# Optimization experiments

Measured on AMD Instinct MI355X. Metric: run time of the kernel, lower is better.

The kernel has to match this reference:

```python
import jax, jax.numpy as jnp
import numpy as np

N_NODES = 50000
N_EDGES = 500000
IN_FEATS = 64
HIDDEN = 64
OUT_FEATS = 8
N_LAYERS = 6
NEG_SLOPE = 0.2
LN_EPS = 1e-5


def setup_inputs() -> dict:
    key = jax.random.key(0)
    ks = jax.random.split(key, 12)
    s_in = 1.0 / np.sqrt(IN_FEATS)
    s_h = 1.0 / np.sqrt(HIDDEN)
    return {
        "nodes": jax.random.normal(ks[0], (N_NODES, IN_FEATS), jnp.float32),
        "src": jax.random.randint(ks[1], (N_EDGES,), 0, N_NODES, jnp.int32),
        "dst": jax.random.randint(ks[2], (N_EDGES,), 0, N_NODES, jnp.int32),
        "w_in": jax.random.normal(ks[3], (IN_FEATS, HIDDEN), jnp.float32) * s_in,
        "b_in": jnp.zeros((HIDDEN,), jnp.float32),
        "w_src": jax.random.normal(ks[4], (N_LAYERS, HIDDEN, HIDDEN), jnp.float32) * s_h,
        "b_src": jnp.zeros((N_LAYERS, HIDDEN), jnp.float32),
        "w_dst": jax.random.normal(ks[5], (N_LAYERS, HIDDEN, HIDDEN), jnp.float32) * s_h,
        "b_dst": jnp.zeros((N_LAYERS, HIDDEN), jnp.float32),
        "attn": jax.random.normal(ks[6], (N_LAYERS, HIDDEN), jnp.float32) * s_h,
        "gamma": jnp.ones((N_LAYERS, HIDDEN), jnp.float32),
        "beta": jnp.zeros((N_LAYERS, HIDDEN), jnp.float32),
        "w_out": jax.random.normal(ks[7], (HIDDEN, OUT_FEATS), jnp.float32) * s_h,
        "b_out": jnp.zeros((OUT_FEATS,), jnp.float32),
    }


def _layernorm(x, g, b):
    m = jnp.mean(x, axis=-1, keepdims=True)
    v = jnp.mean(jnp.square(x - m), axis=-1, keepdims=True)
    return (x - m) * jax.lax.rsqrt(v + LN_EPS) * g + b


def _gatv2(h, src, dst, ws, bs, wd, bd, a, n_nodes):
    # GATv2Conv, num_heads=1 (DGL semantics)
    fs = h @ ws + bs                                  # [N, H] fc_src
    fd = h @ wd + bd                                  # [N, H] fc_dst
    e = jax.nn.leaky_relu(fs[src] + fd[dst], NEG_SLOPE)  # [E, H]
    score = e @ a                                     # [E]
    # segment softmax over incoming edges of each dst node
    mx = jax.ops.segment_max(score, dst, num_segments=n_nodes)
    ex = jnp.exp(score - mx[dst])
    denom = jax.ops.segment_sum(ex, dst, num_segments=n_nodes)
    alpha = ex / denom[dst]                           # [E]
    return jax.ops.segment_sum(alpha[:, None] * fs[src], dst, num_segments=n_nodes)


def reference(nodes, src, dst, w_in, b_in, w_src, b_src, w_dst, b_dst, attn, gamma, beta, w_out, b_out):
    n = nodes.shape[0]
    h = nodes @ w_in + b_in
    for i in range(N_LAYERS):
        t = _gatv2(h, src, dst, w_src[i], b_src[i], w_dst[i], b_dst[i], attn[i], n)
        t = _layernorm(t, gamma[i], beta[i])
        h = h + jax.nn.gelu(t, approximate=False)
    return h @ w_out + b_out
```

## Files before the change

kernel.cpp:

```cpp
#include <hip/hip_runtime.h>
#include <math.h>

#define N_NODES 50000
#define N_EDGES 500000
#define NLAYERS 6
#define NEG_SLOPE 0.2f
#define LN_EPS 1e-5f
#define SCAN_B 1024
#define NSCAN_BLOCKS ((N_NODES + SCAN_B - 1) / SCAN_B)
#define LOG2E 1.4426950408889634f

typedef __attribute__((ext_vector_type(8))) short short8;
typedef __attribute__((ext_vector_type(4))) float f32x4;

__device__ __forceinline__ float wave_sum64(float v) {
#pragma unroll
    for (int m = 32; m >= 1; m >>= 1) v += __shfl_xor(v, m, 64);
    return v;
}

__device__ __forceinline__ int wave_incl_scan(int v, int lane) {
#pragma unroll
    for (int offs = 1; offs < 64; offs <<= 1) {
        int t = __shfl_up(v, offs, 64);
        if (lane >= offs) v += t;
    }
    return v;
}

__device__ __forceinline__ unsigned bf16_rne(float v) {
    unsigned u = __float_as_uint(v);
    return (u + 0x7fffu + ((u >> 16) & 1u)) >> 16;
}

__device__ __forceinline__ float fast_exp2(float x) {
    float r;
    asm("v_exp_f32 %0, %1" : "=v"(r) : "v"(x));
    return r;
}

__global__ void count_deg(const int* __restrict__ dst, int* __restrict__ deg,
                          int* __restrict__ hist) {
    if (blockIdx.x == 0 && threadIdx.x < 64) hist[threadIdx.x] = 0;
    int i = blockIdx.x * blockDim.x + threadIdx.x;
    if (i < N_EDGES) atomicAdd(&deg[dst[i]], 1);
}

__global__ void scan1(const int* __restrict__ deg, int* __restrict__ row_ptr,
                      int* __restrict__ bsum, int* __restrict__ hist) {
    __shared__ int lhist[64];
    __shared__ int wtot[16];
    int t = threadIdx.x;
    if (t < 64) lhist[t] = 0;
    int i = blockIdx.x * SCAN_B + t;
    int lane = t & 63, wv = t >> 6;
    int v = (i < N_NODES) ? deg[i] : 0;
    __syncthreads();
    if (i < N_NODES) atomicAdd(&lhist[min(v, 63)], 1);
    int incl = wave_incl_scan(v, lane);
    if (lane == 63) wtot[wv] = incl;
    __syncthreads();
    if (wv == 0) {
        int wval = (lane < 16) ? wtot[lane] : 0;
        int ws = wave_incl_scan(wval, lane);
        if (lane < 16) wtot[lane] = ws - wval;
    }
    __syncthreads();
    int excl = incl - v + wtot[wv];
    if (i < N_NODES) row_ptr[i] = excl;
    if (t == SCAN_B - 1) bsum[blockIdx.x] = excl + v;
    if (t < 64) atomicAdd(&hist[t], lhist[t]);
}

__global__ void scan3(int* __restrict__ row_ptr, const int* __restrict__ bsum,
                      int* __restrict__ pos, const int* __restrict__ hist,
                      int* __restrict__ binpos) {
    __shared__ int boff_s;
    int t = threadIdx.x;
    if (t < 64) {
        int v = (t < NSCAN_BLOCKS && t < (int)blockIdx.x) ? bsum[t] : 0;
#pragma unroll
        for (int m = 32; m >= 1; m >>= 1) v += __shfl_xor(v, m, 64);
        if (t == 0) boff_s = v;
    }
    if (blockIdx.x == 0 && t >= 64 && t < 128) {
        int lane = t - 64;
        int v = hist[lane];
        int incl = wave_incl_scan(v, lane);
        binpos[lane] = incl - v;
    }
    __syncthreads();
    int i = blockIdx.x * SCAN_B + t;
    if (i < N_NODES) {
        int r = row_ptr[i] + boff_s;
        row_ptr[i] = r;
        pos[i] = r;
    }
    if (i == 0) row_ptr[N_NODES] = N_EDGES;
}

__global__ void bucket_nodes(const int* __restrict__ deg, int* __restrict__ binpos,
                             int* __restrict__ perm) {
    __shared__ int lhist[64], lbase[64];
    int t = threadIdx.x;
    if (t < 64) lhist[t] = 0;
    __syncthreads();
    int i = blockIdx.x * SCAN_B + t;
    int b = 0;
    if (i < N_NODES) {
        b = min(deg[i], 63);
        atomicAdd(&lhist[b], 1);
    }
    __syncthreads();
    if (t < 64) {
        lbase[t] = atomicAdd(&binpos[t], lhist[t]);
        lhist[t] = 0;
    }
    __syncthreads();
    if (i < N_NODES) {
        int r = atomicAdd(&lhist[b], 1);
        perm[lbase[b] + r] = i;
    }
}

__global__ void scatter_edges(const int* __restrict__ dst, const int* __restrict__ src,
                              int* __restrict__ pos, int* __restrict__ srcs) {
    int i = blockIdx.x * blockDim.x + threadIdx.x;
    if (i < N_EDGES) {
        int p = atomicAdd(&pos[dst[i]], 1);
        srcs[p] = src[i];
    }
}

__global__ void pack_w(const float* __restrict__ w_in, const float* __restrict__ w_src,
                       const float* __restrict__ w_dst, unsigned short* __restrict__ wpk_hi,
                       unsigned short* __restrict__ wpk_lo) {
    int b = blockIdx.x;
    const float* W = (b == 0) ? w_in
                              : (b <= 6 ? w_src + (size_t)(b - 1) * 4096
                                        : w_dst + (size_t)(b - 7) * 4096);
    unsigned short* hi = wpk_hi + (size_t)b * 4096;
    unsigned short* lo = wpk_lo + (size_t)b * 4096;
    for (int idx = threadIdx.x; idx < 4096; idx += 256) {
        int t = idx >> 10;
        int s = (idx >> 9) & 1;
        int l = (idx >> 3) & 63;
        int j = idx & 7;
        int row = s * 32 + (l >> 4) * 8 + j;
        int col = t * 16 + (l & 15);
        float v = W[row * 64 + col];
        unsigned rh = bf16_rne(v);
        float hf = __uint_as_float(rh << 16);
        unsigned rl = bf16_rne(v - hf);
        hi[idx] = (unsigned short)rh;
        lo[idx] = (unsigned short)rl;
    }
}

__device__ __forceinline__ void load_split8(const float* __restrict__ p, short8& hi, short8& lo) {
    float4 x0 = *(const float4*)p;
    float4 x1 = *(const float4*)(p + 4);
    float v[8] = {x0.x, x0.y, x0.z, x0.w, x1.x, x1.y, x1.z, x1.w};
#pragma unroll
    for (int j = 0; j < 8; ++j) {
        unsigned rh = bf16_rne(v[j]);
        float hf = __uint_as_float(rh << 16);
        unsigned rl = bf16_rne(v[j] - hf);
        hi[j] = (short)rh;
        lo[j] = (short)rl;
    }
}

__device__ __forceinline__ void mfma_16rows(const short8 ah0, const short8 ah1, const short8 al0,
                                            const short8 al1,
                                            const unsigned short* __restrict__ whi,
                                            const unsigned short* __restrict__ wlo, int lane,
                                            f32x4 acc[4]) {
#pragma unroll
    for (int t = 0; t < 4; ++t) {
#pragma unroll
        for (int s = 0; s < 2; ++s) {
            const size_t boff = ((size_t)((t * 2 + s) * 64 + lane)) * 8;
            short8 bh = *(const short8*)(whi + boff);
            short8 bl = *(const short8*)(wlo + boff);
            short8 a_h = s ? ah1 : ah0;
            short8 a_l = s ? al1 : al0;
            acc[t] = __builtin_amdgcn_mfma_f32_16x16x32_bf16(a_h, bh, acc[t], 0, 0, 0);
            acc[t] = __builtin_amdgcn_mfma_f32_16x16x32_bf16(a_l, bh, acc[t], 0, 0, 0);
            acc[t] = __builtin_amdgcn_mfma_f32_16x16x32_bf16(a_h, bl, acc[t], 0, 0, 0);
        }
    }
}

__global__ void mfma_in_proj(const float* __restrict__ X, const unsigned short* __restrict__ whi,
                             const unsigned short* __restrict__ wlo,
                             const float* __restrict__ bias, float* __restrict__ H) {
    int lane = threadIdx.x & 63, wv = threadIdx.x >> 6;
    int R = blockIdx.x * 64 + wv * 16;
    int arow = min(R + (lane & 15), N_NODES - 1);
    const float* p = X + (size_t)arow * 64 + (lane >> 4) * 8;
    short8 ah0, ah1, al0, al1;
    load_split8(p, ah0, al0);
    load_split8(p + 32, ah1, al1);
    f32x4 acc[4];
    f32x4 z = {0.f, 0.f, 0.f, 0.f};
#pragma unroll
    for (int t = 0; t < 4; ++t) acc[t] = z;
    mfma_16rows(ah0, ah1, al0, al1, whi, wlo, lane, acc);
    int crow = R + (lane >> 4) * 4;
#pragma unroll
    for (int t = 0; t < 4; ++t) {
        int col = t * 16 + (lane & 15);
        float bv = bias[col];
#pragma unroll
        for (int r = 0; r < 4; ++r) {
            int row = crow + r;
            if (row < N_NODES) H[(size_t)row * 64 + col] = acc[t][r] + bv;
        }
    }
}

__global__ void mfma_dual(const float* __restrict__ X, const unsigned short* __restrict__ wshi,
                          const unsigned short* __restrict__ wslo, const float* __restrict__ bs,
                          const unsigned short* __restrict__ wdhi,
                          const unsigned short* __restrict__ wdlo, const float* __restrict__ bd,
                          float* __restrict__ FS, float* __restrict__ FD) {
    int lane = threadIdx.x & 63, wv = threadIdx.x >> 6;
    int R = blockIdx.x * 64 + wv * 16;
    int arow = min(R + (lane & 15), N_NODES - 1);
    const float* p = X + (size_t)arow * 64 + (lane >> 4) * 8;
    short8 ah0, ah1, al0, al1;
    load_split8(p, ah0, al0);
    load_split8(p + 32, ah1, al1);
    f32x4 accS[4], accD[4];
    f32x4 z = {0.f, 0.f, 0.f, 0.f};
#pragma unroll
    for (int t = 0; t < 4; ++t) {
        accS[t] = z;
        accD[t] = z;
    }
    mfma_16rows(ah0, ah1, al0, al1, wshi, wslo, lane, accS);
    mfma_16rows(ah0, ah1, al0, al1, wdhi, wdlo, lane, accD);
    int crow = R + (lane >> 4) * 4;
#pragma unroll
    for (int t = 0; t < 4; ++t) {
        int col = t * 16 + (lane & 15);
        float bsv = bs[col], bdv = bd[col];
#pragma unroll
        for (int r = 0; r < 4; ++r) {
            int row = crow + r;
            if (row < N_NODES) {
                FS[(size_t)row * 64 + col] = accS[t][r] + bsv;
                FD[(size_t)row * 64 + col] = accD[t][r] + bdv;
            }
        }
    }
}

#define WPB 4
__global__ void node_fused_kernel(const float* __restrict__ fs, const float* __restrict__ fd,
                                  const int* __restrict__ row_ptr, const int* __restrict__ srcs,
                                  const int* __restrict__ perm, const float* __restrict__ attn,
                                  const float* __restrict__ gamma, const float* __restrict__ beta,
                                  float* __restrict__ h) {
    __shared__ float xpose[WPB][64];
    int lane = threadIdx.x & 63;
    int wv = threadIdx.x >> 6;
    int q = lane >> 4;
    int ql = lane & 15;
    int f0 = ql << 2;
    int idx = blockIdx.x * WPB + wv;
    if (idx >= N_NODES) return;
    int n = perm[idx];
    float gL = gamma[lane], bL = beta[lane];
    float hval = h[(size_t)n * 64 + lane];
    float4 a4 = *(const float4*)&attn[f0];
    a4.x *= LOG2E;
    a4.y *= LOG2E;
    a4.z *= LOG2E;
    a4.w *= LOG2E;
    int beg = row_ptr[n], end = row_ptr[n + 1];
    int deg = end - beg;
    float4 fd4 = *(const float4*)&fd[(size_t)n * 64 + f0];
    float d = 0.f;
    float4 acc = make_float4(0.f, 0.f, 0.f, 0.f);
    for (int c0 = 0; c0 < deg; c0 += 64) {
        int cl = min(64, deg - c0);
        int sv = (lane < cl) ? srcs[beg + c0 + lane] : 0;
        int nt = (cl + 3) >> 2;
        float4 rowA = make_float4(0.f, 0.f, 0.f, 0.f), rowB = rowA;
        int sid0 = __shfl(sv, q, 64);
        if (q < cl) rowA = *(const float4*)&fs[(size_t)sid0 * 64 + f0];
        int sid1 = __shfl(sv, (4 + q) & 63, 64);
        if (4 + q < cl) rowB = *(const float4*)&fs[(size_t)sid1 * 64 + f0];
        for (int t = 0; t < nt; ++t) {
            int eoff = 4 * t + q;
            bool valid = eoff < cl;
            float4 cur = rowA;
            rowA = rowB;
            int e2 = 4 * (t + 2) + q;
            int sid2 = __shfl(sv, e2 & 63, 64);
            if (e2 < cl) rowB = *(const float4*)&fs[(size_t)sid2 * 64 + f0];
            float vx = cur.x + fd4.x, vy = cur.y + fd4.y;
            float vz = cur.z + fd4.z, vw = cur.w + fd4.w;
            vx = fmaxf(vx, NEG_SLOPE * vx);
            vy = fmaxf(vy, NEG_SLOPE * vy);
            vz = fmaxf(vz, NEG_SLOPE * vz);
            vw = fmaxf(vw, NEG_SLOPE * vw);
            float sp = fmaf(a4.x, vx, fmaf(a4.y, vy, fmaf(a4.z, vz, a4.w * vw)));
            sp += __shfl_xor(sp, 1, 64);
            sp += __shfl_xor(sp, 2, 64);
            sp += __shfl_xor(sp, 4, 64);
            sp += __shfl_xor(sp, 8, 64);
            float w = valid ? fast_exp2(sp) : 0.f;
            d += w;
            acc.x = fmaf(w, cur.x, acc.x);
            acc.y = fmaf(w, cur.y, acc.y);
            acc.z = fmaf(w, cur.z, acc.z);
            acc.w = fmaf(w, cur.w, acc.w);
        }
    }
    d += __shfl_xor(d, 16, 64);
    d += __shfl_xor(d, 32, 64);
    acc.x += __shfl_xor(acc.x, 16, 64);
    acc.y += __shfl_xor(acc.y, 16, 64);
    acc.z += __shfl_xor(acc.z, 16, 64);
    acc.w += __shfl_xor(acc.w, 16, 64);
    acc.x += __shfl_xor(acc.x, 32, 64);
    acc.y += __shfl_xor(acc.y, 32, 64);
    acc.z += __shfl_xor(acc.z, 32, 64);
    acc.w += __shfl_xor(acc.w, 32, 64);
    float inv = (d > 0.f) ? 1.f / d : 0.f;
    acc.x *= inv;
    acc.y *= inv;
    acc.z *= inv;
    acc.w *= inv;
    if (q == 0) *(float4*)&xpose[wv][f0] = acc;
    float val = xpose[wv][lane];
    float mean = wave_sum64(val) * 0.015625f;
    float dev = val - mean;
    float var = wave_sum64(dev * dev) * 0.015625f;
    float rstd = rsqrtf(var + LN_EPS);
    float tval = fmaf(dev * rstd, gL, bL);
    float g = 0.5f * tval * (1.f + erff(tval * 0.70710678118654752f));
    h[(size_t)n * 64 + lane] = hval + g;
}

__global__ void out_proj_kernel(const float* __restrict__ h, const float* __restrict__ W,
                                const float* __restrict__ b, float* __restrict__ out) {
    __shared__ float Ws[64 * 8];
    __shared__ float bs[8];
    __shared__ float Hs[32][65];
    int t = threadIdx.x;
    for (int i = t; i < 512; i += 256) Ws[i] = W[i];
    if (t < 8) bs[t] = b[t];
    int n0 = blockIdx.x * 32;
    for (int i = t; i < 32 * 64; i += 256) {
        int r = i >> 6, c = i & 63;
        int n = n0 + r;
        Hs[r][c] = (n < N_NODES) ? h[(size_t)n * 64 + c] : 0.f;
    }
    __syncthreads();
    int nl = t >> 3, o = t & 7;
    int n = n0 + nl;
    if (n >= N_NODES) return;
    float acc = bs[o];
#pragma unroll
    for (int k = 0; k < 64; ++k) acc = fmaf(Hs[nl][k], Ws[k * 8 + o], acc);
    out[(size_t)n * 8 + o] = acc;
}

extern "C" void kernel_launch(void* const* d_in, const int* in_sizes, int n_in,
                              void* d_out, int out_size, void* d_ws, size_t ws_size,
                              hipStream_t stream) {
    const float* nodes = (const float*)d_in[0];
    const int* src = (const int*)d_in[1];
    const int* dst = (const int*)d_in[2];
    const float* w_in = (const float*)d_in[3];
    const float* b_in = (const float*)d_in[4];
    const float* w_src = (const float*)d_in[5];
    const float* b_src = (const float*)d_in[6];
    const float* w_dst = (const float*)d_in[7];
    const float* b_dst = (const float*)d_in[8];
    const float* attn = (const float*)d_in[9];
    const float* gamma = (const float*)d_in[10];
    const float* beta = (const float*)d_in[11];
    const float* w_out = (const float*)d_in[12];
    const float* b_out = (const float*)d_in[13];
    float* out = (float*)d_out;

    char* ws = (char*)d_ws;
    size_t off = 0;
    auto alloc = [&](size_t bytes) {
        void* p = ws + off;
        off += (bytes + 255) & ~(size_t)255;
        return p;
    };
    float* h = (float*)alloc((size_t)N_NODES * 64 * 4);
    float* fs = (float*)alloc((size_t)N_NODES * 64 * 4);
    float* fd = (float*)alloc((size_t)N_NODES * 64 * 4);
    unsigned short* wpk_hi = (unsigned short*)alloc((size_t)13 * 4096 * 2);
    unsigned short* wpk_lo = (unsigned short*)alloc((size_t)13 * 4096 * 2);
    int* deg = (int*)alloc((size_t)N_NODES * 4);
    int* row_ptr = (int*)alloc((size_t)(N_NODES + 1) * 4);
    int* pos = (int*)alloc((size_t)N_NODES * 4);
    int* srcs = (int*)alloc((size_t)N_EDGES * 4);
    int* bsum = (int*)alloc((size_t)NSCAN_BLOCKS * 4);
    int* hist = (int*)alloc((size_t)64 * 4);
    int* binpos = (int*)alloc((size_t)64 * 4);
    int* perm = (int*)alloc((size_t)N_NODES * 4);

    hipMemsetAsync(deg, 0, (size_t)N_NODES * 4, stream);
    count_deg<<<(N_EDGES + 255) / 256, 256, 0, stream>>>(dst, deg, hist);
    scan1<<<NSCAN_BLOCKS, SCAN_B, 0, stream>>>(deg, row_ptr, bsum, hist);
    scan3<<<NSCAN_BLOCKS, SCAN_B, 0, stream>>>(row_ptr, bsum, pos, hist, binpos);
    bucket_nodes<<<NSCAN_BLOCKS, SCAN_B, 0, stream>>>(deg, binpos, perm);
    scatter_edges<<<(N_EDGES + 255) / 256, 256, 0, stream>>>(dst, src, pos, srcs);

    pack_w<<<13, 256, 0, stream>>>(w_in, w_src, w_dst, wpk_hi, wpk_lo);

    mfma_in_proj<<<(N_NODES + 63) / 64, 256, 0, stream>>>(nodes, wpk_hi, wpk_lo, b_in, h);

    for (int l = 0; l < NLAYERS; ++l) {
        mfma_dual<<<(N_NODES + 63) / 64, 256, 0, stream>>>(
            h, wpk_hi + (size_t)(1 + l) * 4096, wpk_lo + (size_t)(1 + l) * 4096,
            b_src + (size_t)l * 64, wpk_hi + (size_t)(7 + l) * 4096,
            wpk_lo + (size_t)(7 + l) * 4096, b_dst + (size_t)l * 64, fs, fd);
        node_fused_kernel<<<(N_NODES + WPB - 1) / WPB, 256, 0, stream>>>(
            fs, fd, row_ptr, srcs, perm, attn + (size_t)l * 64, gamma + (size_t)l * 64,
            beta + (size_t)l * 64, h);
    }

    out_proj_kernel<<<(N_NODES + 31) / 32, 256, 0, stream>>>(h, w_out, b_out, out);
}
```

Before: 352.5 us.

## Process two degree-sorted nodes per wave with DPP row reductions

```diff
diff --git a/kernel.cpp b/kernel.cpp
--- a/kernel.cpp
+++ b/kernel.cpp
@@ -16,6 +16,29 @@
 __device__ __forceinline__ float wave_sum64(float v) {
 #pragma unroll
     for (int m = 32; m >= 1; m >>= 1) v += __shfl_xor(v, m, 64);
+    return v;
+}
+
+__device__ __forceinline__ float dpp_rowsum16(float v) {
+    int x = __float_as_int(v);
+    int y = __builtin_amdgcn_update_dpp(x, x, 0x121, 0xf, 0xf, false);
+    v += __int_as_float(y);
+    x = __float_as_int(v);
+    y = __builtin_amdgcn_update_dpp(x, x, 0x122, 0xf, 0xf, false);
+    v += __int_as_float(y);
+    x = __float_as_int(v);
+    y = __builtin_amdgcn_update_dpp(x, x, 0x124, 0xf, 0xf, false);
+    v += __int_as_float(y);
+    x = __float_as_int(v);
+    y = __builtin_amdgcn_update_dpp(x, x, 0x128, 0xf, 0xf, false);
+    v += __int_as_float(y);
+    return v;
+}
+
+__device__ __forceinline__ float wave_sum64_fast(float v) {
+    v = dpp_rowsum16(v);
+    v += __shfl_xor(v, 16, 64);
+    v += __shfl_xor(v, 32, 64);
     return v;
 }
 
@@ -56,7 +79,7 @@
     int lane = t & 63, wv = t >> 6;
     int v = (i < N_NODES) ? deg[i] : 0;
     __syncthreads();
-    if (i < N_NODES) atomicAdd(&lhist[min(v, 63)], 1);
+    if (i < N_NODES) atomicAdd(&lhist[63 - min(v, 63)], 1);
     int incl = wave_incl_scan(v, lane);
     if (lane == 63) wtot[wv] = incl;
     __syncthreads();
@@ -108,7 +131,7 @@
     int i = blockIdx.x * SCAN_B + t;
     int b = 0;
     if (i < N_NODES) {
-        b = min(deg[i], 63);
+        b = 63 - min(deg[i], 63);
         atomicAdd(&lhist[b], 1);
     }
     __syncthreads();
@@ -263,87 +286,131 @@
                                   const int* __restrict__ perm, const float* __restrict__ attn,
                                   const float* __restrict__ gamma, const float* __restrict__ beta,
                                   float* __restrict__ h) {
-    __shared__ float xpose[WPB][64];
+    __shared__ float xpose[WPB][2][64];
     int lane = threadIdx.x & 63;
     int wv = threadIdx.x >> 6;
     int q = lane >> 4;
     int ql = lane & 15;
     int f0 = ql << 2;
-    int idx = blockIdx.x * WPB + wv;
-    if (idx >= N_NODES) return;
-    int n = perm[idx];
+    int gw = blockIdx.x * WPB + wv;
+    int iA = gw * 2;
+    if (iA >= N_NODES) return;
+    int iB = iA + 1;
+    bool hasB = iB < N_NODES;
+    int nA = perm[iA];
+    int nB = hasB ? perm[iB] : nA;
     float gL = gamma[lane], bL = beta[lane];
-    float hval = h[(size_t)n * 64 + lane];
+    float hvalA = h[(size_t)nA * 64 + lane];
+    float hvalB = h[(size_t)nB * 64 + lane];
     float4 a4 = *(const float4*)&attn[f0];
     a4.x *= LOG2E;
     a4.y *= LOG2E;
     a4.z *= LOG2E;
     a4.w *= LOG2E;
-    int beg = row_ptr[n], end = row_ptr[n + 1];
-    int deg = end - beg;
-    float4 fd4 = *(const float4*)&fd[(size_t)n * 64 + f0];
-    float d = 0.f;
-    float4 acc = make_float4(0.f, 0.f, 0.f, 0.f);
-    for (int c0 = 0; c0 < deg; c0 += 64) {
-        int cl = min(64, deg - c0);
-        int sv = (lane < cl) ? srcs[beg + c0 + lane] : 0;
-        int nt = (cl + 3) >> 2;
-        float4 rowA = make_float4(0.f, 0.f, 0.f, 0.f), rowB = rowA;
-        int sid0 = __shfl(sv, q, 64);
-        if (q < cl) rowA = *(const float4*)&fs[(size_t)sid0 * 64 + f0];
-        int sid1 = __shfl(sv, (4 + q) & 63, 64);
-        if (4 + q < cl) rowB = *(const float4*)&fs[(size_t)sid1 * 64 + f0];
-        for (int t = 0; t < nt; ++t) {
+    int begA = row_ptr[nA], degA = row_ptr[nA + 1] - begA;
+    int begB = row_ptr[nB], degB = row_ptr[nB + 1] - begB;
+    float4 fdA = *(const float4*)&fd[(size_t)nA * 64 + f0];
+    float4 fdB = *(const float4*)&fd[(size_t)nB * 64 + f0];
+    float dA = 0.f, dB = 0.f;
+    float4 accA = make_float4(0.f, 0.f, 0.f, 0.f), accB = accA;
+    int degM = max(degA, degB);
+    for (int c0 = 0; c0 < degM; c0 += 64) {
+        int clA = min(64, degA - c0);
+        int clB = min(64, degB - c0);
+        int svA = (lane < clA) ? srcs[begA + c0 + lane] : 0;
+        int svB = (lane < clB) ? srcs[begB + c0 + lane] : 0;
+        int ntm = (max(clA, clB) + 3) >> 2;
+        float4 zf = make_float4(0.f, 0.f, 0.f, 0.f);
+        float4 rA0 = zf, rA1 = zf, rB0 = zf, rB1 = zf;
+        int sA0 = __shfl(svA, q, 64);
+        if (q < clA) rA0 = *(const float4*)&fs[(size_t)sA0 * 64 + f0];
+        int sB0 = __shfl(svB, q, 64);
+        if (q < clB) rB0 = *(const float4*)&fs[(size_t)sB0 * 64 + f0];
+        int sA1 = __shfl(svA, (4 + q) & 63, 64);
+        if (4 + q < clA) rA1 = *(const float4*)&fs[(size_t)sA1 * 64 + f0];
+        int sB1 = __shfl(svB, (4 + q) & 63, 64);
+        if (4 + q < clB) rB1 = *(const float4*)&fs[(size_t)sB1 * 64 + f0];
+        for (int t = 0; t < ntm; ++t) {
             int eoff = 4 * t + q;
-            bool valid = eoff < cl;
-            float4 cur = rowA;
-            rowA = rowB;
+            bool vA = eoff < clA, vB = eoff < clB;
+            float4 cA = rA0, cB = rB0;
+            rA0 = rA1;
+            rB0 = rB1;
             int e2 = 4 * (t + 2) + q;
-            int sid2 = __shfl(sv, e2 & 63, 64);
-            if (e2 < cl) rowB = *(const float4*)&fs[(size_t)sid2 * 64 + f0];
-            float vx = cur.x + fd4.x, vy = cur.y + fd4.y;
-            float vz = cur.z + fd4.z, vw = cur.w + fd4.w;
-            vx = fmaxf(vx, NEG_SLOPE * vx);
-            vy = fmaxf(vy, NEG_SLOPE * vy);
-            vz = fmaxf(vz, NEG_SLOPE * vz);
-            vw = fmaxf(vw, NEG_SLOPE * vw);
-            float sp = fmaf(a4.x, vx, fmaf(a4.y, vy, fmaf(a4.z, vz, a4.w * vw)));
-            sp += __shfl_xor(sp, 1, 64);
-            sp += __shfl_xor(sp, 2, 64);
-            sp += __shfl_xor(sp, 4, 64);
-            sp += __shfl_xor(sp, 8, 64);
-            float w = valid ? fast_exp2(sp) : 0.f;
-            d += w;
-            acc.x = fmaf(w, cur.x, acc.x);
-            acc.y = fmaf(w, cur.y, acc.y);
-            acc.z = fmaf(w, cur.z, acc.z);
-            acc.w = fmaf(w, cur.w, acc.w);
+            int sA2 = __shfl(svA, e2 & 63, 64);
+            int sB2 = __shfl(svB, e2 & 63, 64);
+            rA1 = zf;
+            rB1 = zf;
+            if (e2 < clA) rA1 = *(const float4*)&fs[(size_t)sA2 * 64 + f0];
+            if (e2 < clB) rB1 = *(const float4*)&fs[(size_t)sB2 * 64 + f0];
+            float ax = cA.x + fdA.x, ay = cA.y + fdA.y, az = cA.z + fdA.z, aw = cA.w + fdA.w;
+            float bx = cB.x + fdB.x, by = cB.y + fdB.y, bz = cB.z + fdB.z, bw = cB.w + fdB.w;
+            ax = fmaxf(ax, NEG_SLOPE * ax);
+            ay = fmaxf(ay, NEG_SLOPE * ay);
+            az = fmaxf(az, NEG_SLOPE * az);
+            aw = fmaxf(aw, NEG_SLOPE * aw);
+            bx = fmaxf(bx, NEG_SLOPE * bx);
+            by = fmaxf(by, NEG_SLOPE * by);
+            bz = fmaxf(bz, NEG_SLOPE * bz);
+            bw = fmaxf(bw, NEG_SLOPE * bw);
+            float spA = fmaf(a4.x, ax, fmaf(a4.y, ay, fmaf(a4.z, az, a4.w * aw)));
+            float spB = fmaf(a4.x, bx, fmaf(a4.y, by, fmaf(a4.z, bz, a4.w * bw)));
+            spA = dpp_rowsum16(spA);
+            spB = dpp_rowsum16(spB);
+            float wA = vA ? fast_exp2(spA) : 0.f;
+            float wB = vB ? fast_exp2(spB) : 0.f;
+            dA += wA;
+            dB += wB;
+            accA.x = fmaf(wA, cA.x, accA.x);
+            accA.y = fmaf(wA, cA.y, accA.y);
+            accA.z = fmaf(wA, cA.z, accA.z);
+            accA.w = fmaf(wA, cA.w, accA.w);
+            accB.x = fmaf(wB, cB.x, accB.x);
+            accB.y = fmaf(wB, cB.y, accB.y);
+            accB.z = fmaf(wB, cB.z, accB.z);
+            accB.w = fmaf(wB, cB.w, accB.w);
         }
     }
-    d += __shfl_xor(d, 16, 64);
-    d += __shfl_xor(d, 32, 64);
-    acc.x += __shfl_xor(acc.x, 16, 64);
-    acc.y += __shfl_xor(acc.y, 16, 64);
-    acc.z += __shfl_xor(acc.z, 16, 64);
-    acc.w += __shfl_xor(acc.w, 16, 64);
-    acc.x += __shfl_xor(acc.x, 32, 64);
-    acc.y += __shfl_xor(acc.y, 32, 64);
-    acc.z += __shfl_xor(acc.z, 32, 64);
-    acc.w += __shfl_xor(acc.w, 32, 64);
-    float inv = (d > 0.f) ? 1.f / d : 0.f;
-    acc.x *= inv;
-    acc.y *= inv;
-    acc.z *= inv;
-    acc.w *= inv;
-    if (q == 0) *(float4*)&xpose[wv][f0] = acc;
-    float val = xpose[wv][lane];
-    float mean = wave_sum64(val) * 0.015625f;
-    float dev = val - mean;
-    float var = wave_sum64(dev * dev) * 0.015625f;
-    float rstd = rsqrtf(var + LN_EPS);
-    float tval = fmaf(dev * rstd, gL, bL);
-    float g = 0.5f * tval * (1.f + erff(tval * 0.70710678118654752f));
-    h[(size_t)n * 64 + lane] = hval + g;
+#pragma unroll
+    for (int msk = 16; msk <= 32; msk <<= 1) {
+        dA += __shfl_xor(dA, msk, 64);
+        dB += __shfl_xor(dB, msk, 64);
+        accA.x += __shfl_xor(accA.x, msk, 64);
+        accA.y += __shfl_xor(accA.y, msk, 64);
+        accA.z += __shfl_xor(accA.z, msk, 64);
+        accA.w += __shfl_xor(accA.w, msk, 64);
+        accB.x += __shfl_xor(accB.x, msk, 64);
+        accB.y += __shfl_xor(accB.y, msk, 64);
+        accB.z += __shfl_xor(accB.z, msk, 64);
+        accB.w += __shfl_xor(accB.w, msk, 64);
+    }
+    float invA = (dA > 0.f) ? 1.f / dA : 0.f;
+    float invB = (dB > 0.f) ? 1.f / dB : 0.f;
+    accA.x *= invA;
+    accA.y *= invA;
+    accA.z *= invA;
+    accA.w *= invA;
+    accB.x *= invB;
+    accB.y *= invB;
+    accB.z *= invB;
+    accB.w *= invB;
+    if (q == 0) *(float4*)&xpose[wv][0][f0] = accA;
+    if (q == 1) *(float4*)&xpose[wv][1][f0] = accB;
+    float valA = xpose[wv][0][lane];
+    float valB = xpose[wv][1][lane];
+    float meanA = wave_sum64_fast(valA) * 0.015625f;
+    float meanB = wave_sum64_fast(valB) * 0.015625f;
+    float devA = valA - meanA, devB = valB - meanB;
+    float varA = wave_sum64_fast(devA * devA) * 0.015625f;
+    float varB = wave_sum64_fast(devB * devB) * 0.015625f;
+    float rstdA = rsqrtf(varA + LN_EPS), rstdB = rsqrtf(varB + LN_EPS);
+    float tA = fmaf(devA * rstdA, gL, bL);
+    float tB = fmaf(devB * rstdB, gL, bL);
+    const float IS2 = 0.70710678118654752f;
+    float gA = 0.5f * tA * (1.f + erff(tA * IS2));
+    float gB = 0.5f * tB * (1.f + erff(tB * IS2));
+    h[(size_t)nA * 64 + lane] = hvalA + gA;
+    if (hasB) h[(size_t)nB * 64 + lane] = hvalB + gB;
 }
 
 __global__ void out_proj_kernel(const float* __restrict__ h, const float* __restrict__ W,
@@ -421,12 +488,13 @@
 
     mfma_in_proj<<<(N_NODES + 63) / 64, 256, 0, stream>>>(nodes, wpk_hi, wpk_lo, b_in, h);
 
+    const int NF_GRID = (N_NODES + WPB * 2 - 1) / (WPB * 2);
     for (int l = 0; l < NLAYERS; ++l) {
         mfma_dual<<<(N_NODES + 63) / 64, 256, 0, stream>>>(
             h, wpk_hi + (size_t)(1 + l) * 4096, wpk_lo + (size_t)(1 + l) * 4096,
             b_src + (size_t)l * 64, wpk_hi + (size_t)(7 + l) * 4096,
             wpk_lo + (size_t)(7 + l) * 4096, b_dst + (size_t)l * 64, fs, fd);
-        node_fused_kernel<<<(N_NODES + WPB - 1) / WPB, 256, 0, stream>>>(
+        node_fused_kernel<<<NF_GRID, 256, 0, stream>>>(
             fs, fd, row_ptr, srcs, perm, attn + (size_t)l * 64, gamma + (size_t)l * 64,
             beta + (size_t)l * 64, h);
     }
```

Measured after the change: 356.7 us. No clear change (+1.2%).
